# Optimization experiments

Measured on AMD Instinct MI355X. Metric: run time of the kernel, lower is better.

## Reference

```python
import jax, jax.numpy as jnp
import numpy as np

N = 12288   # num_nodes
D = 128     # isize
K_TOP = 31  # k + 1, per top_k(similarities, self.k + 1)


def setup_inputs() -> dict:
    key = jax.random.key(0)
    features = jax.random.normal(key, (N, D), dtype=jnp.float32)
    eye = jnp.eye(D, dtype=jnp.float32)  # param_init: weight <- I, bias <- 0
    return {
        "features": features,
        "W1": eye,
        "b1": jnp.zeros((D,), jnp.float32),
        "W2": eye,
        "b2": jnp.zeros((D,), jnp.float32),
    }


def reference(features, W1, b1, W2, b2):
    # internal_forward: Linear -> ReLU -> Linear (nlayers=2, act='relu')
    h = jax.nn.relu(features @ W1.T + b1)
    h = h @ W2.T + b2
    # F.normalize(h, dim=1, p=2) with eps=1e-12
    hn = h / jnp.maximum(jnp.linalg.norm(h, axis=1, keepdims=True), 1e-12)
    # dense N x N cosine similarity
    sim = hn @ hn.T
    # top_k: keep top (k+1) entries per row, zero elsewhere; then apply_non_linearity='relu'
    vals, idx = jax.lax.top_k(sim, K_TOP)          # [N, K_TOP]
    rows = jnp.arange(sim.shape[0])[:, None]       # [N, 1]
    # relu(sim * mask) == scatter relu(top-k values) into a zero matrix
    out = jnp.zeros_like(sim).at[rows, idx].set(jax.nn.relu(vals))
    return out
```

## Files before the change

### kernel.cpp

```cpp
#include <hip/hip_runtime.h>
#include <stdint.h>
#include <math.h>

#define NN 12288
#define DD 128
#define KTOP 31
#define TCAND 64
#define CCAP 128
#define RPB 48
#define WPL 16
#define NIT 24
#define KPROW 1024

typedef __attribute__((ext_vector_type(8))) short bf16x8;
typedef __attribute__((ext_vector_type(4))) float f32x4;

__device__ __forceinline__ unsigned short f2bf(float x) {
  unsigned int u = __float_as_uint(x);
  u += 0x7fffu + ((u >> 16) & 1u);
  return (unsigned short)(u >> 16);
}

__device__ __forceinline__ unsigned umed3(unsigned a, unsigned b, unsigned c) {
  unsigned d;
  asm("v_med3_u32 %0, %1, %2, %3" : "=v"(d) : "v"(a), "v"(b), "v"(c));
  return d;
}

#define PINS8(Lx, P) { \
  const unsigned p_ = (P); \
  _Pragma("unroll") \
  for (int i_ = 0; i_ < 7; ++i_) \
    Lx[i_] = umed3(p_, Lx[i_], Lx[i_ + 1]); \
  Lx[7] = Lx[7] > p_ ? Lx[7] : p_; }

#define LKEY(ACC, LX, COLBASE) { \
  _Pragma("unroll") \
  for (int r_ = 0; r_ < 4; ++r_) { \
    unsigned bf_ = f2bf((ACC)[r_]); \
    unsigned s_ = (bf_ & 0x8000u) ? 0u : bf_; \
    unsigned p_k = (s_ << 16) | (unsigned)((COLBASE) + quad * 4 + r_); \
    PINS8(LX, p_k) } }

__global__ __launch_bounds__(128)
void wtrans_kernel(const float* __restrict__ W1, const float* __restrict__ W2,
                   float* __restrict__ W1T, float* __restrict__ W2T) {
  const int r = blockIdx.x, c = threadIdx.x;
  W1T[(size_t)c * DD + r] = W1[(size_t)r * DD + c];
  W2T[(size_t)c * DD + r] = W2[(size_t)r * DD + c];
}

__global__ __launch_bounds__(256)
void mlp_norm_kernel(const float* __restrict__ feat,
                     const float* __restrict__ W1T, const float* __restrict__ b1,
                     const float* __restrict__ W2T, const float* __restrict__ b2,
                     double* __restrict__ hn64, unsigned short* __restrict__ hnb) {
  __shared__ float  bufA[16][DD];
  __shared__ double bufB[16][DD];
  __shared__ double bufC[16][DD];
  __shared__ double mnorm[16];
  const int t = threadIdx.x;
  const int c = t & 127;
  const int g = t >> 7;
  const int row0 = blockIdx.x * 16 + g * 8;

  #pragma unroll
  for (int rr = 0; rr < 8; ++rr)
    bufA[g * 8 + rr][c] = feat[(size_t)(row0 + rr) * DD + c];
  __syncthreads();

  {
    double acc[8] = {0,0,0,0,0,0,0,0};
    for (int k = 0; k < DD; k += 4) {
      double w0 = (double)W1T[(size_t)k * DD + c];
      double w1 = (double)W1T[(size_t)(k + 1) * DD + c];
      double w2 = (double)W1T[(size_t)(k + 2) * DD + c];
      double w3 = (double)W1T[(size_t)(k + 3) * DD + c];
      #pragma unroll
      for (int rr = 0; rr < 8; ++rr) {
        f32x4 a4 = *(const f32x4*)(&bufA[g * 8 + rr][k]);
        acc[rr] = fma(w0, (double)a4.x, acc[rr]);
        acc[rr] = fma(w1, (double)a4.y, acc[rr]);
        acc[rr] = fma(w2, (double)a4.z, acc[rr]);
        acc[rr] = fma(w3, (double)a4.w, acc[rr]);
      }
    }
    double bb = (double)b1[c];
    #pragma unroll
    for (int rr = 0; rr < 8; ++rr)
      bufB[g * 8 + rr][c] = fmax(acc[rr] + bb, 0.0);
  }
  __syncthreads();
  {
    double acc[8] = {0,0,0,0,0,0,0,0};
    for (int k = 0; k < DD; k += 2) {
      double w0 = (double)W2T[(size_t)k * DD + c];
      double w1 = (double)W2T[(size_t)(k + 1) * DD + c];
      #pragma unroll
      for (int rr = 0; rr < 8; ++rr) {
        double2 a2 = *(const double2*)(&bufB[g * 8 + rr][k]);
        acc[rr] = fma(w0, a2.x, acc[rr]);
        acc[rr] = fma(w1, a2.y, acc[rr]);
      }
    }
    double bb = (double)b2[c];
    #pragma unroll
    for (int rr = 0; rr < 8; ++rr)
      bufC[g * 8 + rr][c] = acc[rr] + bb;
  }
  __syncthreads();

  const int lane = t & 63;
  const int w = t >> 6;
  #pragma unroll
  for (int r2 = 0; r2 < 4; ++r2) {
    int rr = w * 4 + r2;
    double x0 = bufC[rr][lane];
    double x1 = bufC[rr][lane + 64];
    double s = x0 * x0 + x1 * x1;
    #pragma unroll
    for (int d = 1; d < 64; d <<= 1)
      s += __shfl_xor(s, d);
    if (lane == 0) mnorm[rr] = fmax(sqrt(s), 1e-12);
  }
  __syncthreads();
  #pragma unroll
  for (int rr = 0; rr < 8; ++rr) {
    double v = bufC[g * 8 + rr][c] / mnorm[g * 8 + rr];
    hn64[(size_t)(row0 + rr) * DD + c] = v;
    hnb[(size_t)(row0 + rr) * DD + c] = f2bf((float)v);
  }
}

__global__ __launch_bounds__(1024)
void simloop_kernel(const unsigned short* __restrict__ hnb,
                    float* __restrict__ out) {
  const int t = threadIdx.x, lane = t & 63, wv = t >> 6;
  const int m = lane & 15, quad = lane >> 4;
  const int row0 = blockIdx.x * RPB;
  const int it0 = (int)(((blockIdx.x >> 3) * 3u) % NIT);

  bf16x8 af0[4], af1[4], af2[4];
  #pragma unroll
  for (int kc = 0; kc < 4; ++kc) {
    af0[kc] = *(const bf16x8*)(hnb + (size_t)(row0 + m) * DD + kc * 32 + quad * 8);
    af1[kc] = *(const bf16x8*)(hnb + (size_t)(row0 + 16 + m) * DD + kc * 32 + quad * 8);
    af2[kc] = *(const bf16x8*)(hnb + (size_t)(row0 + 32 + m) * DD + kc * 32 + quad * 8);
  }

  unsigned LA0[8] = {0,0,0,0,0,0,0,0}, LB0[8] = {0,0,0,0,0,0,0,0};
  unsigned LA1[8] = {0,0,0,0,0,0,0,0}, LB1[8] = {0,0,0,0,0,0,0,0};
  unsigned LA2[8] = {0,0,0,0,0,0,0,0}, LB2[8] = {0,0,0,0,0,0,0,0};

  f32x4* outz = (f32x4*)(out + (size_t)row0 * NN);
  const f32x4 z = {0.0f, 0.0f, 0.0f, 0.0f};

  for (int itt = 0; itt < NIT; ++itt) {
    int it = itt + it0; if (it >= NIT) it -= NIT;
    const int cb = it * (WPL * 32) + wv * 32;
    f32x4 a00 = {0,0,0,0}, a01 = {0,0,0,0};
    f32x4 a10 = {0,0,0,0}, a11 = {0,0,0,0};
    f32x4 a20 = {0,0,0,0}, a21 = {0,0,0,0};
    #pragma unroll
    for (int kc = 0; kc < 4; ++kc) {
      bf16x8 b0 = *(const bf16x8*)(hnb + (size_t)(cb + m) * DD + kc * 32 + quad * 8);
      bf16x8 b1 = *(const bf16x8*)(hnb + (size_t)(cb + 16 + m) * DD + kc * 32 + quad * 8);
      a00 = __builtin_amdgcn_mfma_f32_16x16x32_bf16(b0, af0[kc], a00, 0, 0, 0);
      a01 = __builtin_amdgcn_mfma_f32_16x16x32_bf16(b1, af0[kc], a01, 0, 0, 0);
      a10 = __builtin_amdgcn_mfma_f32_16x16x32_bf16(b0, af1[kc], a10, 0, 0, 0);
      a11 = __builtin_amdgcn_mfma_f32_16x16x32_bf16(b1, af1[kc], a11, 0, 0, 0);
      a20 = __builtin_amdgcn_mfma_f32_16x16x32_bf16(b0, af2[kc], a20, 0, 0, 0);
      a21 = __builtin_amdgcn_mfma_f32_16x16x32_bf16(b1, af2[kc], a21, 0, 0, 0);
    }
    #pragma unroll
    for (int j = 0; j < 6; ++j)
      __builtin_nontemporal_store(z, &outz[it * 6144 + j * 1024 + t]);
    LKEY(a00, LA0, cb)      LKEY(a01, LB0, cb + 16)
    LKEY(a10, LA1, cb)      LKEY(a11, LB1, cb + 16)
    LKEY(a20, LA2, cb)      LKEY(a21, LB2, cb + 16)
  }

  asm volatile("s_waitcnt vmcnt(0)" ::: "memory");
  __syncthreads();

  const int sbase = (wv * 4 + quad) * 16;
  {
    unsigned* d0 = (unsigned*)(out + (size_t)(row0 + m) * NN) + sbase;
    *(uint4*)(d0)     = make_uint4(LA0[0], LA0[1], LA0[2], LA0[3]);
    *(uint4*)(d0 + 4) = make_uint4(LA0[4], LA0[5], LA0[6], LA0[7]);
    *(uint4*)(d0 + 8) = make_uint4(LB0[0], LB0[1], LB0[2], LB0[3]);
    *(uint4*)(d0 + 12)= make_uint4(LB0[4], LB0[5], LB0[6], LB0[7]);
    unsigned* d1 = (unsigned*)(out + (size_t)(row0 + 16 + m) * NN) + sbase;
    *(uint4*)(d1)     = make_uint4(LA1[0], LA1[1], LA1[2], LA1[3]);
    *(uint4*)(d1 + 4) = make_uint4(LA1[4], LA1[5], LA1[6], LA1[7]);
    *(uint4*)(d1 + 8) = make_uint4(LB1[0], LB1[1], LB1[2], LB1[3]);
    *(uint4*)(d1 + 12)= make_uint4(LB1[4], LB1[5], LB1[6], LB1[7]);
    unsigned* d2 = (unsigned*)(out + (size_t)(row0 + 32 + m) * NN) + sbase;
    *(uint4*)(d2)     = make_uint4(LA2[0], LA2[1], LA2[2], LA2[3]);
    *(uint4*)(d2 + 4) = make_uint4(LA2[4], LA2[5], LA2[6], LA2[7]);
    *(uint4*)(d2 + 8) = make_uint4(LB2[0], LB2[1], LB2[2], LB2[3]);
    *(uint4*)(d2 + 12)= make_uint4(LB2[4], LB2[5], LB2[6], LB2[7]);
  }
}

__global__ __launch_bounds__(256)
void select_kernel(const double* __restrict__ hn64, float* __restrict__ out) {
  __shared__ unsigned scand[4][CCAP];
  __shared__ double cres[4][CCAP];
  const int t = threadIdx.x, lane = t & 63, wv = t >> 6;
  const int row = blockIdx.x * 4 + wv;
  float* orow = out + (size_t)row * NN;

  unsigned k16[16];
  {
    const unsigned* src = (const unsigned*)orow + lane * 16;
    #pragma unroll
    for (int q = 0; q < 4; ++q) {
      uint4 a = *(const uint4*)(src + q * 4);
      k16[q * 4 + 0] = a.x; k16[q * 4 + 1] = a.y;
      k16[q * 4 + 2] = a.z; k16[q * 4 + 3] = a.w;
    }
  }

  unsigned lo = 0, hi = 0xFFFFu;
  while (lo < hi) {
    unsigned mid = (lo + hi + 1) >> 1;
    int c = 0;
    #pragma unroll
    for (int i = 0; i < 16; ++i) c += (int)((k16[i] >> 16) >= mid);
    #pragma unroll
    for (int d = 1; d < 64; d <<= 1) c += __shfl_xor(c, d);
    if (c >= TCAND) lo = mid; else hi = mid - 1;
  }
  const unsigned thr = lo;

  int cl = 0;
  #pragma unroll
  for (int i = 0; i < 16; ++i) cl += (int)((k16[i] >> 16) >= thr);
  int pre = cl;
  #pragma unroll
  for (int d = 1; d < 64; d <<= 1) {
    int y = __shfl_up(pre, d);
    if (lane >= d) pre += y;
  }
  const int total = __shfl(pre, 63);
  const int nc = total < CCAP ? total : CCAP;
  int slot = pre - cl;
  #pragma unroll
  for (int i = 0; i < 16; ++i) {
    if ((k16[i] >> 16) >= thr) {
      if (slot < CCAP) scand[wv][slot] = k16[i];
      ++slot;
    }
  }

  const double* arow = hn64 + (size_t)row * DD;
  const int g4 = lane >> 4;
  const int kl = (lane & 15) * 8;
  double a[8];
  #pragma unroll
  for (int i = 0; i < 8; ++i) a[i] = arow[kl + i];
  const int ng = (nc + 7) >> 3;
  for (int g = 0; g < ng; ++g) {
    const int ci0 = 8 * g + g4;
    const int ci1 = ci0 + 4;
    double p0 = 0.0, p1 = 0.0;
    if (ci0 < nc) {
      const int col = (int)(scand[wv][ci0] & 0xFFFFu);
      const double* brow = hn64 + (size_t)col * DD + kl;
      double2 b01 = *(const double2*)(brow);
      double2 b23 = *(const double2*)(brow + 2);
      double2 b45 = *(const double2*)(brow + 4);
      double2 b67 = *(const double2*)(brow + 6);
      p0 = fma(a[0], b01.x, fma(a[1], b01.y, fma(a[2], b23.x, a[3] * b23.y)));
      p0 = fma(a[4], b45.x, fma(a[5], b45.y, fma(a[6], b67.x, fma(a[7], b67.y, p0))));
    }
    if (ci1 < nc) {
      const int col = (int)(scand[wv][ci1] & 0xFFFFu);
      const double* brow = hn64 + (size_t)col * DD + kl;
      double2 b01 = *(const double2*)(brow);
      double2 b23 = *(const double2*)(brow + 2);
      double2 b45 = *(const double2*)(brow + 4);
      double2 b67 = *(const double2*)(brow + 6);
      p1 = fma(a[0], b01.x, fma(a[1], b01.y, fma(a[2], b23.x, a[3] * b23.y)));
      p1 = fma(a[4], b45.x, fma(a[5], b45.y, fma(a[6], b67.x, fma(a[7], b67.y, p1))));
    }
    #pragma unroll
    for (int d = 1; d < 16; d <<= 1) {
      p0 += __shfl_xor(p0, d);
      p1 += __shfl_xor(p1, d);
    }
    if ((lane & 15) == 0) {
      if (ci0 < nc) cres[wv][ci0] = p0;
      if (ci1 < nc) cres[wv][ci1] = p1;
    }
  }
  double rv0 = -1.0e300, rv1 = -1.0e300;
  int rc0 = 0x7fffffff, rc1 = 0x7fffffff;
  if (lane < nc)      { rv0 = cres[wv][lane];      rc0 = (int)(scand[wv][lane] & 0xFFFFu); }
  if (lane + 64 < nc) { rv1 = cres[wv][lane + 64]; rc1 = (int)(scand[wv][lane + 64] & 0xFFFFu); }

  float fkv = 0.0f; int fkc = 0;
  for (int itk = 0; itk < KTOP; ++itk) {
    bool f = (rv0 > rv1) || (rv0 == rv1 && rc0 < rc1);
    double bv = f ? rv0 : rv1;
    int bc = f ? rc0 : rc1;
    #pragma unroll
    for (int d = 1; d < 64; d <<= 1) {
      double ov = __shfl_xor(bv, d);
      int    oc = __shfl_xor(bc, d);
      bool tk = (ov > bv) || (ov == bv && oc < bc);
      bv = tk ? ov : bv;
      bc = tk ? oc : bc;
    }
    if (lane == itk) { fkv = (float)fmax(bv, 0.0); fkc = bc; }
    if (rv0 == bv && rc0 == bc) rv0 = -1.0e300;
    else if (rv1 == bv && rc1 == bc) rv1 = -1.0e300;
  }

  {
    f32x4* zp = (f32x4*)orow;
    const f32x4 z = {0.0f, 0.0f, 0.0f, 0.0f};
    #pragma unroll
    for (int j = 0; j < 4; ++j)
      __builtin_nontemporal_store(z, &zp[j * 64 + lane]);
  }
  asm volatile("s_waitcnt vmcnt(0)" ::: "memory");
  if (lane < KTOP) orow[fkc] = fkv;
}

extern "C" void kernel_launch(void* const* d_in, const int* in_sizes, int n_in,
                              void* d_out, int out_size, void* d_ws, size_t ws_size,
                              hipStream_t stream) {
  const float* feat = (const float*)d_in[0];
  const float* W1 = (const float*)d_in[1];
  const float* b1 = (const float*)d_in[2];
  const float* W2 = (const float*)d_in[3];
  const float* b2 = (const float*)d_in[4];
  float* out = (float*)d_out;

  double* hn64 = (double*)d_ws;
  unsigned short* hnb = (unsigned short*)(hn64 + (size_t)NN * DD);
  float* W1T = (float*)(hnb + (size_t)NN * DD);
  float* W2T = W1T + DD * DD;

  wtrans_kernel<<<DD, DD, 0, stream>>>(W1, W2, W1T, W2T);
  mlp_norm_kernel<<<NN / 16, 256, 0, stream>>>(feat, W1T, b1, W2T, b2, hn64, hnb);
  simloop_kernel<<<NN / RPB, 1024, 0, stream>>>(hnb, out);
  select_kernel<<<NN / 4, 256, 0, stream>>>(hn64, out);
}
```

Baseline: 882.9 us.

## Fuse top-k selection into similarity kernel via shared-memory key staging

Merges the selection kernel into the similarity kernel. Per-lane candidate keys are staged in a padded shared-memory buffer instead of being written to the output rows and read back by a second launch. Each of the 16 waves then runs the threshold search, fp64 rescoring and final top-k for one row, in three passes over the 48-row tile. This removes a global round trip of keys, one kernel launch, and the re-zeroing of the first 1024 columns of every row. In exchange, the rescoring and selection now run serially inside the MFMA kernel with about 86KB of LDS per block, which may reduce occupancy and overlap.

```diff
diff --git a/kernel.cpp b/kernel.cpp
--- a/kernel.cpp
+++ b/kernel.cpp
@@ -10,7 +10,7 @@
 #define RPB 48
 #define WPL 16
 #define NIT 24
-#define KPROW 1024
+#define KBS 1028
 
 typedef __attribute__((ext_vector_type(8))) short bf16x8;
 typedef __attribute__((ext_vector_type(4))) float f32x4;
@@ -41,6 +41,13 @@
     unsigned s_ = (bf_ & 0x8000u) ? 0u : bf_; \
     unsigned p_k = (s_ << 16) | (unsigned)((COLBASE) + quad * 4 + r_); \
     PINS8(LX, p_k) } }
+
+#define KDUMP(LAx, LBx) { \
+  unsigned* d_ = &keybuf[m][(wv * 4 + quad) * 16]; \
+  *(uint4*)(d_)      = make_uint4(LAx[0], LAx[1], LAx[2], LAx[3]); \
+  *(uint4*)(d_ + 4)  = make_uint4(LAx[4], LAx[5], LAx[6], LAx[7]); \
+  *(uint4*)(d_ + 8)  = make_uint4(LBx[0], LBx[1], LBx[2], LBx[3]); \
+  *(uint4*)(d_ + 12) = make_uint4(LBx[4], LBx[5], LBx[6], LBx[7]); }
 
 __global__ __launch_bounds__(128)
 void wtrans_kernel(const float* __restrict__ W1, const float* __restrict__ W2,
@@ -133,8 +140,12 @@
 }
 
 __global__ __launch_bounds__(1024)
-void simloop_kernel(const unsigned short* __restrict__ hnb,
-                    float* __restrict__ out) {
+void simsel_kernel(const unsigned short* __restrict__ hnb,
+                   const double* __restrict__ hn64,
+                   float* __restrict__ out) {
+  __shared__ unsigned keybuf[16][KBS];
+  __shared__ unsigned scand[WPL][CCAP];
+  __shared__ double cres[WPL][CCAP];
   const int t = threadIdx.x, lane = t & 63, wv = t >> 6;
   const int m = lane & 15, quad = lane >> 4;
   const int row0 = blockIdx.x * RPB;
@@ -183,150 +194,117 @@
   asm volatile("s_waitcnt vmcnt(0)" ::: "memory");
   __syncthreads();
 
-  const int sbase = (wv * 4 + quad) * 16;
-  {
-    unsigned* d0 = (unsigned*)(out + (size_t)(row0 + m) * NN) + sbase;
-    *(uint4*)(d0)     = make_uint4(LA0[0], LA0[1], LA0[2], LA0[3]);
-    *(uint4*)(d0 + 4) = make_uint4(LA0[4], LA0[5], LA0[6], LA0[7]);
-    *(uint4*)(d0 + 8) = make_uint4(LB0[0], LB0[1], LB0[2], LB0[3]);
-    *(uint4*)(d0 + 12)= make_uint4(LB0[4], LB0[5], LB0[6], LB0[7]);
-    unsigned* d1 = (unsigned*)(out + (size_t)(row0 + 16 + m) * NN) + sbase;
-    *(uint4*)(d1)     = make_uint4(LA1[0], LA1[1], LA1[2], LA1[3]);
-    *(uint4*)(d1 + 4) = make_uint4(LA1[4], LA1[5], LA1[6], LA1[7]);
-    *(uint4*)(d1 + 8) = make_uint4(LB1[0], LB1[1], LB1[2], LB1[3]);
-    *(uint4*)(d1 + 12)= make_uint4(LB1[4], LB1[5], LB1[6], LB1[7]);
-    unsigned* d2 = (unsigned*)(out + (size_t)(row0 + 32 + m) * NN) + sbase;
-    *(uint4*)(d2)     = make_uint4(LA2[0], LA2[1], LA2[2], LA2[3]);
-    *(uint4*)(d2 + 4) = make_uint4(LA2[4], LA2[5], LA2[6], LA2[7]);
-    *(uint4*)(d2 + 8) = make_uint4(LB2[0], LB2[1], LB2[2], LB2[3]);
-    *(uint4*)(d2 + 12)= make_uint4(LB2[4], LB2[5], LB2[6], LB2[7]);
-  }
-}
-
-__global__ __launch_bounds__(256)
-void select_kernel(const double* __restrict__ hn64, float* __restrict__ out) {
-  __shared__ unsigned scand[4][CCAP];
-  __shared__ double cres[4][CCAP];
-  const int t = threadIdx.x, lane = t & 63, wv = t >> 6;
-  const int row = blockIdx.x * 4 + wv;
-  float* orow = out + (size_t)row * NN;
-
-  unsigned k16[16];
-  {
-    const unsigned* src = (const unsigned*)orow + lane * 16;
-    #pragma unroll
-    for (int q = 0; q < 4; ++q) {
-      uint4 a = *(const uint4*)(src + q * 4);
-      k16[q * 4 + 0] = a.x; k16[q * 4 + 1] = a.y;
-      k16[q * 4 + 2] = a.z; k16[q * 4 + 3] = a.w;
-    }
-  }
-
-  unsigned lo = 0, hi = 0xFFFFu;
-  while (lo < hi) {
-    unsigned mid = (lo + hi + 1) >> 1;
-    int c = 0;
-    #pragma unroll
-    for (int i = 0; i < 16; ++i) c += (int)((k16[i] >> 16) >= mid);
-    #pragma unroll
-    for (int d = 1; d < 64; d <<= 1) c += __shfl_xor(c, d);
-    if (c >= TCAND) lo = mid; else hi = mid - 1;
-  }
-  const unsigned thr = lo;
-
-  int cl = 0;
-  #pragma unroll
-  for (int i = 0; i < 16; ++i) cl += (int)((k16[i] >> 16) >= thr);
-  int pre = cl;
-  #pragma unroll
-  for (int d = 1; d < 64; d <<= 1) {
-    int y = __shfl_up(pre, d);
-    if (lane >= d) pre += y;
-  }
-  const int total = __shfl(pre, 63);
-  const int nc = total < CCAP ? total : CCAP;
-  int slot = pre - cl;
-  #pragma unroll
-  for (int i = 0; i < 16; ++i) {
-    if ((k16[i] >> 16) >= thr) {
-      if (slot < CCAP) scand[wv][slot] = k16[i];
-      ++slot;
-    }
-  }
-
-  const double* arow = hn64 + (size_t)row * DD;
-  const int g4 = lane >> 4;
-  const int kl = (lane & 15) * 8;
-  double a[8];
-  #pragma unroll
-  for (int i = 0; i < 8; ++i) a[i] = arow[kl + i];
-  const int ng = (nc + 7) >> 3;
-  for (int g = 0; g < ng; ++g) {
-    const int ci0 = 8 * g + g4;
-    const int ci1 = ci0 + 4;
-    double p0 = 0.0, p1 = 0.0;
-    if (ci0 < nc) {
-      const int col = (int)(scand[wv][ci0] & 0xFFFFu);
-      const double* brow = hn64 + (size_t)col * DD + kl;
-      double2 b01 = *(const double2*)(brow);
-      double2 b23 = *(const double2*)(brow + 2);
-      double2 b45 = *(const double2*)(brow + 4);
-      double2 b67 = *(const double2*)(brow + 6);
-      p0 = fma(a[0], b01.x, fma(a[1], b01.y, fma(a[2], b23.x, a[3] * b23.y)));
-      p0 = fma(a[4], b45.x, fma(a[5], b45.y, fma(a[6], b67.x, fma(a[7], b67.y, p0))));
-    }
-    if (ci1 < nc) {
-      const int col = (int)(scand[wv][ci1] & 0xFFFFu);
-      const double* brow = hn64 + (size_t)col * DD + kl;
-      double2 b01 = *(const double2*)(brow);
-      double2 b23 = *(const double2*)(brow + 2);
-      double2 b45 = *(const double2*)(brow + 4);
-      double2 b67 = *(const double2*)(brow + 6);
-      p1 = fma(a[0], b01.x, fma(a[1], b01.y, fma(a[2], b23.x, a[3] * b23.y)));
-      p1 = fma(a[4], b45.x, fma(a[5], b45.y, fma(a[6], b67.x, fma(a[7], b67.y, p1))));
-    }
-    #pragma unroll
-    for (int d = 1; d < 16; d <<= 1) {
-      p0 += __shfl_xor(p0, d);
-      p1 += __shfl_xor(p1, d);
-    }
-    if ((lane & 15) == 0) {
-      if (ci0 < nc) cres[wv][ci0] = p0;
-      if (ci1 < nc) cres[wv][ci1] = p1;
-    }
-  }
-  double rv0 = -1.0e300, rv1 = -1.0e300;
-  int rc0 = 0x7fffffff, rc1 = 0x7fffffff;
-  if (lane < nc)      { rv0 = cres[wv][lane];      rc0 = (int)(scand[wv][lane] & 0xFFFFu); }
-  if (lane + 64 < nc) { rv1 = cres[wv][lane + 64]; rc1 = (int)(scand[wv][lane + 64] & 0xFFFFu); }
-
-  float fkv = 0.0f; int fkc = 0;
-  for (int itk = 0; itk < KTOP; ++itk) {
-    bool f = (rv0 > rv1) || (rv0 == rv1 && rc0 < rc1);
-    double bv = f ? rv0 : rv1;
-    int bc = f ? rc0 : rc1;
+  #pragma unroll
+  for (int p = 0; p < 3; ++p) {
+    if (p == 0)      { KDUMP(LA0, LB0) }
+    else if (p == 1) { KDUMP(LA1, LB1) }
+    else             { KDUMP(LA2, LB2) }
+    __syncthreads();
+
+    const int grow = row0 + p * 16 + wv;
+    unsigned k16[16];
+    #pragma unroll
+    for (int i = 0; i < 16; ++i)
+      k16[i] = keybuf[wv][i * 64 + lane];
+
+    unsigned lo = 0, hi = 0xFFFFu;
+    while (lo < hi) {
+      unsigned mid = (lo + hi + 1) >> 1;
+      int c = 0;
+      #pragma unroll
+      for (int i = 0; i < 16; ++i) c += (int)((k16[i] >> 16) >= mid);
+      #pragma unroll
+      for (int d = 1; d < 64; d <<= 1) c += __shfl_xor(c, d);
+      if (c >= TCAND) lo = mid; else hi = mid - 1;
+    }
+    const unsigned thr = lo;
+
+    int cl = 0;
+    #pragma unroll
+    for (int i = 0; i < 16; ++i) cl += (int)((k16[i] >> 16) >= thr);
+    int pre = cl;
     #pragma unroll
     for (int d = 1; d < 64; d <<= 1) {
-      double ov = __shfl_xor(bv, d);
-      int    oc = __shfl_xor(bc, d);
-      bool tk = (ov > bv) || (ov == bv && oc < bc);
-      bv = tk ? ov : bv;
-      bc = tk ? oc : bc;
-    }
-    if (lane == itk) { fkv = (float)fmax(bv, 0.0); fkc = bc; }
-    if (rv0 == bv && rc0 == bc) rv0 = -1.0e300;
-    else if (rv1 == bv && rc1 == bc) rv1 = -1.0e300;
-  }
-
-  {
-    f32x4* zp = (f32x4*)orow;
-    const f32x4 z = {0.0f, 0.0f, 0.0f, 0.0f};
-    #pragma unroll
-    for (int j = 0; j < 4; ++j)
-      __builtin_nontemporal_store(z, &zp[j * 64 + lane]);
-  }
-  asm volatile("s_waitcnt vmcnt(0)" ::: "memory");
-  if (lane < KTOP) orow[fkc] = fkv;
+      int y = __shfl_up(pre, d);
+      if (lane >= d) pre += y;
+    }
+    const int total = __shfl(pre, 63);
+    const int nc = total < CCAP ? total : CCAP;
+    int slot = pre - cl;
+    #pragma unroll
+    for (int i = 0; i < 16; ++i) {
+      if ((k16[i] >> 16) >= thr) {
+        if (slot < CCAP) scand[wv][slot] = k16[i];
+        ++slot;
+      }
+    }
+
+    const double* arow = hn64 + (size_t)grow * DD;
+    const int g4 = lane >> 4;
+    const int kl = (lane & 15) * 8;
+    double a[8];
+    #pragma unroll
+    for (int i = 0; i < 8; ++i) a[i] = arow[kl + i];
+    const int ng = (nc + 7) >> 3;
+    for (int g = 0; g < ng; ++g) {
+      const int ci0 = 8 * g + g4;
+      const int ci1 = ci0 + 4;
+      double p0 = 0.0, p1 = 0.0;
+      if (ci0 < nc) {
+        const int col = (int)(scand[wv][ci0] & 0xFFFFu);
+        const double* brow = hn64 + (size_t)col * DD + kl;
+        double2 b01 = *(const double2*)(brow);
+        double2 b23 = *(const double2*)(brow + 2);
+        double2 b45 = *(const double2*)(brow + 4);
+        double2 b67 = *(const double2*)(brow + 6);
+        p0 = fma(a[0], b01.x, fma(a[1], b01.y, fma(a[2], b23.x, a[3] * b23.y)));
+        p0 = fma(a[4], b45.x, fma(a[5], b45.y, fma(a[6], b67.x, fma(a[7], b67.y, p0))));
+      }
+      if (ci1 < nc) {
+        const int col = (int)(scand[wv][ci1] & 0xFFFFu);
+        const double* brow = hn64 + (size_t)col * DD + kl;
+        double2 b01 = *(const double2*)(brow);
+        double2 b23 = *(const double2*)(brow + 2);
+        double2 b45 = *(const double2*)(brow + 4);
+        double2 b67 = *(const double2*)(brow + 6);
+        p1 = fma(a[0], b01.x, fma(a[1], b01.y, fma(a[2], b23.x, a[3] * b23.y)));
+        p1 = fma(a[4], b45.x, fma(a[5], b45.y, fma(a[6], b67.x, fma(a[7], b67.y, p1))));
+      }
+      #pragma unroll
+      for (int d = 1; d < 16; d <<= 1) {
+        p0 += __shfl_xor(p0, d);
+        p1 += __shfl_xor(p1, d);
+      }
+      if ((lane & 15) == 0) {
+        if (ci0 < nc) cres[wv][ci0] = p0;
+        if (ci1 < nc) cres[wv][ci1] = p1;
+      }
+    }
+    double rv0 = -1.0e300, rv1 = -1.0e300;
+    int rc0 = 0x7fffffff, rc1 = 0x7fffffff;
+    if (lane < nc)      { rv0 = cres[wv][lane];      rc0 = (int)(scand[wv][lane] & 0xFFFFu); }
+    if (lane + 64 < nc) { rv1 = cres[wv][lane + 64]; rc1 = (int)(scand[wv][lane + 64] & 0xFFFFu); }
+
+    float fkv = 0.0f; int fkc = 0;
+    for (int itk = 0; itk < KTOP; ++itk) {
+      bool f = (rv0 > rv1) || (rv0 == rv1 && rc0 < rc1);
+      double bv = f ? rv0 : rv1;
+      int bc = f ? rc0 : rc1;
+      #pragma unroll
+      for (int d = 1; d < 64; d <<= 1) {
+        double ov = __shfl_xor(bv, d);
+        int    oc = __shfl_xor(bc, d);
+        bool tk = (ov > bv) || (ov == bv && oc < bc);
+        bv = tk ? ov : bv;
+        bc = tk ? oc : bc;
+      }
+      if (lane == itk) { fkv = (float)fmax(bv, 0.0); fkc = bc; }
+      if (rv0 == bv && rc0 == bc) rv0 = -1.0e300;
+      else if (rv1 == bv && rc1 == bc) rv1 = -1.0e300;
+    }
+    if (lane < KTOP) out[(size_t)grow * NN + fkc] = fkv;
+    __syncthreads();
+  }
 }
 
 extern "C" void kernel_launch(void* const* d_in, const int* in_sizes, int n_in,
@@ -346,6 +324,5 @@
 
   wtrans_kernel<<<DD, DD, 0, stream>>>(W1, W2, W1T, W2T);
   mlp_norm_kernel<<<NN / 16, 256, 0, stream>>>(feat, W1T, b1, W2T, b2, hn64, hnb);
-  simloop_kernel<<<NN / RPB, 1024, 0, stream>>>(hnb, out);
-  select_kernel<<<NN / 4, 256, 0, stream>>>(hn64, out);
-}
+  simsel_kernel<<<NN / RPB, 1024, 0, stream>>>(hnb, hn64, out);
+}
```

Result: no change. 896.3 us (+1.5%).
